# Performance work log

Hardware: AMD Instinct MI355X
Metric: run time of the kernel (lower is better)

## Reference

```python
import jax, jax.numpy as jnp
import numpy as np
from jax import lax

B, T = 512, 64
IN, H, V1, P = 256, 512, 101, 8  # input_size, rnn_size, vocab_size+1, max_param
CLS, REG = 512, 512


def setup_inputs() -> dict:
    key = jax.random.key(0)
    ks = jax.random.split(key, 20)
    u = lambda k, s: jax.random.uniform(k, s, jnp.float32, -0.1, 0.1)
    sh = 1.0 / np.sqrt(H)
    ul = lambda k, s: jax.random.uniform(k, s, jnp.float32, -sh, sh)
    return {
        "x": jax.random.normal(ks[0], (B, IN), jnp.float32),
        "y": jax.random.randint(ks[1], (B, T), 0, V1),
        "embed": u(ks[2], (V1, IN)),
        "w_ih0": ul(ks[3], (4 * H, IN)),
        "w_hh0": ul(ks[4], (4 * H, H)),
        "w_ih1": ul(ks[5], (4 * H, H)),
        "w_hh1": ul(ks[6], (4 * H, H)),
        "l1w": u(ks[7], (CLS, H)), "l1b": jnp.zeros((CLS,), jnp.float32),
        "l2w": u(ks[8], (V1, CLS)), "l2b": jnp.zeros((V1,), jnp.float32),
        "r1w": u(ks[9], (REG, H)), "r1b": jnp.zeros((REG,), jnp.float32),
        "r2w": u(ks[10], (V1 * P, V1 + REG)), "r2b": jnp.zeros((V1 * P,), jnp.float32),
    }


def _cell(xi, h, c, wih, whh):
    g = xi @ wih.T + h @ whh.T          # [B, 4H], gate order i,f,g,o (no bias)
    i, f, gg, o = jnp.split(g, 4, axis=-1)
    c = jax.nn.sigmoid(f) * c + jax.nn.sigmoid(i) * jnp.tanh(gg)
    h = jax.nn.sigmoid(o) * jnp.tanh(c)
    return h, c


def reference(x, y, embed, w_ih0, w_hh0, w_ih1, w_hh1,
              l1w, l1b, l2w, l2b, r1w, r1b, r2w, r2b):
    # teacher forcing (sample_prob=0): step-0 input is x, step-i input is embed(y[:, i-1])
    emb = embed[y[:, :-1]]                                  # [B, T-1, IN]
    xt = jnp.concatenate([x[None], jnp.transpose(emb, (1, 0, 2))], axis=0)  # [T, B, IN]

    z = jnp.zeros((x.shape[0], H), x.dtype)

    def step(carry, xi):
        h0, c0, h1, c1 = carry
        h0, c0 = _cell(xi, h0, c0, w_ih0, w_hh0)
        h1, c1 = _cell(h0, h1, c1, w_ih1, w_hh1)
        return (h0, c0, h1, c1), h1

    _, outs = lax.scan(step, (z, z, z, z), xt)              # [T, B, H]

    feat2 = jax.nn.relu(outs @ l1w.T + l1b) @ l2w.T + l2b   # [T, B, V1]
    pgm_score = jax.nn.log_softmax(feat2, axis=-1)
    trans_prob = lax.stop_gradient(jax.nn.softmax(feat2, axis=-1))
    pf1 = jax.nn.relu(outs @ r1w.T + r1b)                   # [T, B, REG]
    ps = (jnp.concatenate([trans_prob, pf1], axis=-1) @ r2w.T + r2b)
    ps = ps.reshape(T, -1, V1, P)                           # [T, B, V1, P]
    idx = y.T                                               # [T, B]
    param = ps[jnp.arange(T)[:, None], jnp.arange(x.shape[0])[None, :], idx]  # [T, B, P]
    return (jnp.transpose(pgm_score, (1, 0, 2)),            # [B, T, V1]
            jnp.transpose(param, (1, 0, 2)))                # [B, T, P]
```

## Files before the change

kernel.cpp:

```cpp
#include <hip/hip_runtime.h>
#include <stdint.h>

typedef unsigned short u16;
typedef short bf16x8 __attribute__((ext_vector_type(8)));
typedef float f32x4 __attribute__((ext_vector_type(4)));
typedef int i32x4 __attribute__((ext_vector_type(4)));

#define DEV static __device__ __forceinline__

constexpr int B_ = 512, T_ = 64, IN_ = 256, H_ = 512, V1_ = 101, P_ = 8, G4_ = 2048;
constexpr int EXR = 613;
constexpr int M_  = T_ * B_;
constexpr int NBLK = 256;

DEV float b2f(u16 u) { union { uint32_t i; float f; } v; v.i = ((uint32_t)u) << 16; return v.f; }
DEV u16 f2b(float f) {
  union { float f; uint32_t i; } v; v.f = f;
  uint32_t i = v.i;
  return (u16)((i + 0x7fffu + ((i >> 16) & 1u)) >> 16);
}
DEV float sigf(float x) { return 1.f / (1.f + __expf(-x)); }
DEV float tanh_(float x) {
  float c = fminf(fmaxf(x, -15.f), 15.f);
  float e = __expf(2.f * c);
  return (e - 1.f) / (e + 1.f);
}
DEV bf16x8 ld8(const u16* p) { return *reinterpret_cast<const bf16x8*>(p); }
DEV f32x4 mfma16(bf16x8 a, bf16x8 b, f32x4 c) {
  return __builtin_amdgcn_mfma_f32_16x16x32_bf16(a, b, c, 0, 0, 0);
}

struct CvtArgs {
  const float* src[9];
  u16* dst[9];
  int pre[10];
};

__global__ __launch_bounds__(256) void k_cvtall(CvtArgs a) {
  int gid = blockIdx.x * 256 + threadIdx.x;
  if (gid >= a.pre[9]) return;
  int s = 0;
#pragma unroll
  for (int i = 1; i < 9; ++i) s += (gid >= a.pre[i]);
  const int local = gid - a.pre[s];
  const float4 v = reinterpret_cast<const float4*>(a.src[s])[local];
  ushort4 o;
  o.x = f2b(v.x); o.y = f2b(v.y); o.z = f2b(v.z); o.w = f2b(v.w);
  reinterpret_cast<ushort4*>(a.dst[s])[local] = o;
}

__global__ __launch_bounds__(256) void k_precomp(const u16* __restrict__ ex_src,
                                                 const u16* __restrict__ wih0b,
                                                 float* __restrict__ EX0) {
  const int lane = threadIdx.x & 63;
  const int wv = threadIdx.x >> 6;
  const int m0 = blockIdx.x * 64 + wv * 16;
  const int n0 = blockIdx.y * 64;
  const int lr = lane & 15;
  const int lk = (lane >> 4) * 8;

  const int arow = m0 + lr;
  const bool valid = arow < EXR;

  f32x4 acc[4] = {};
  for (int k0 = 0; k0 < IN_; k0 += 32) {
    bf16x8 a = {};
    if (valid) a = ld8(ex_src + (size_t)arow * IN_ + k0 + lk);
#pragma unroll
    for (int c = 0; c < 4; ++c) {
      bf16x8 b = ld8(wih0b + (size_t)(n0 + c * 16 + lr) * IN_ + k0 + lk);
      acc[c] = mfma16(a, b, acc[c]);
    }
  }
  const int rb = (lane >> 4) * 4;
#pragma unroll
  for (int c = 0; c < 4; ++c)
#pragma unroll
    for (int r = 0; r < 4; ++r) {
      int row = m0 + rb + r;
      int col = n0 + c * 16 + (lane & 15);
      if (row < EXR) EX0[(size_t)row * G4_ + col] = acc[c][r];
    }
}

__global__ __launch_bounds__(512, 1) void k_scan(
    const u16* __restrict__ whh0, const u16* __restrict__ wih1, const u16* __restrict__ whh1,
    const float* __restrict__ EX0, const int* __restrict__ y,
    u16* h0buf, u16* h1buf, unsigned* flags ) {
  __shared__ u16 h0s[16 * 512];
  __shared__ u16 h1s[16 * 512];
  __shared__ u16 stage0[16][64];
  __shared__ u16 stage1[16][64];
  const size_t BH = (size_t)B_ * H_;
  const int tid = threadIdx.x;
  const int lane = tid & 63;
  const int wv = tid >> 6;
  const int q = wv & 3;
  const bool isL1 = wv >= 4;
  const int bm = blockIdx.x >> 3;
  const int bj = blockIdx.x & 7;
  const int lr = lane & 15;
  const int lk = (lane >> 4) * 8;
  const int col = bj * 64 + q * 16 + lr;
  const int rb = (lane >> 4) * 4;
  const int lcol = q * 16 + lr;

  const u16* wp[8];
#pragma unroll
  for (int g = 0; g < 4; ++g) {
    if (!isL1) {
      wp[g] = whh0 + (size_t)(g * H_ + col) * H_ + lk;
      wp[4 + g] = whh0 + (size_t)(g * H_ + col) * H_ + lk;
    } else {
      wp[g] = wih1 + (size_t)(g * H_ + col) * H_ + lk;
      wp[4 + g] = whh1 + (size_t)(g * H_ + col) * H_ + lk;
    }
  }
  f32x4 cst = {};
  unsigned* gflags = flags + bm * 16;

  for (int k = 0; k <= T_; ++k) {
    {
      const u16* h0g = h0buf + (size_t)k * BH + (size_t)(bm * 16) * H_;
#pragma unroll
      for (int rr = 0; rr < 2; ++rr) {
        const int idx = rr * 512 + tid;
        const int row = idx >> 6, cc = idx & 63;
        i32x4 d = *(const i32x4*)(h0g + (size_t)row * H_ + cc * 8);
        *(i32x4*)((char*)h0s + row * 1024 + ((cc * 16) ^ ((row & 7) << 4))) = d;
      }
      if (k >= 1) {
        const u16* h1g = h1buf + (size_t)(k - 1) * BH + (size_t)(bm * 16) * H_;
#pragma unroll
        for (int rr = 0; rr < 2; ++rr) {
          const int idx = rr * 512 + tid;
          const int row = idx >> 6, cc = idx & 63;
          i32x4 d = *(const i32x4*)(h1g + (size_t)row * H_ + cc * 8);
          *(i32x4*)((char*)h1s + row * 1024 + ((cc * 16) ^ ((row & 7) << 4))) = d;
        }
      }
    }
    __syncthreads();

    if (!isL1) {
      if (k < T_) {
        float ex[4][4];
#pragma unroll
        for (int r = 0; r < 4; ++r) {
          const int row = bm * 16 + rb + r;
          const int srow = (k == 0) ? (V1_ + row) : y[row * T_ + k - 1];
          const float* bp = EX0 + (size_t)srow * G4_ + col;
#pragma unroll
          for (int g = 0; g < 4; ++g) ex[g][r] = bp[(size_t)g * H_];
        }
        bf16x8 wf[4];
#pragma unroll
        for (int g = 0; g < 4; ++g) wf[g] = ld8(wp[g]);
        f32x4 acc[4] = {};
#pragma unroll
        for (int i = 0; i < 16; ++i) {
          bf16x8 a0 = *(const bf16x8*)((const char*)h0s + lr * 1024 + (((i * 32 + lk) * 2) ^ ((lr & 7) << 4)));
          bf16x8 nf[4];
#pragma unroll
          for (int g = 0; g < 4; ++g) nf[g] = (i < 15) ? ld8(wp[g] + (i + 1) * 32) : wf[g];
#pragma unroll
          for (int g = 0; g < 4; ++g) acc[g] = mfma16(a0, wf[g], acc[g]);
#pragma unroll
          for (int g = 0; g < 4; ++g) wf[g] = nf[g];
        }
#pragma unroll
        for (int r = 0; r < 4; ++r) {
          float iv = acc[0][r] + ex[0][r], fv = acc[1][r] + ex[1][r];
          float gv = acc[2][r] + ex[2][r], ov = acc[3][r] + ex[3][r];
          float cn = sigf(fv) * cst[r] + sigf(iv) * tanh_(gv);
          cst[r] = cn;
          stage0[rb + r][lcol] = f2b(sigf(ov) * tanh_(cn));
        }
      }
    } else {
      if (k >= 1) {
        bf16x8 wfa[4], wfb[4];
#pragma unroll
        for (int g = 0; g < 4; ++g) { wfa[g] = ld8(wp[g]); wfb[g] = ld8(wp[4 + g]); }
        f32x4 acc[4] = {};
#pragma unroll
        for (int i = 0; i < 16; ++i) {
          const int so = ((i * 32 + lk) * 2) ^ ((lr & 7) << 4);
          bf16x8 a0 = *(const bf16x8*)((const char*)h0s + lr * 1024 + so);
          bf16x8 a1 = *(const bf16x8*)((const char*)h1s + lr * 1024 + so);
          bf16x8 nfa[4], nfb[4];
#pragma unroll
          for (int g = 0; g < 4; ++g) {
            nfa[g] = (i < 15) ? ld8(wp[g] + (i + 1) * 32) : wfa[g];
            nfb[g] = (i < 15) ? ld8(wp[4 + g] + (i + 1) * 32) : wfb[g];
          }
#pragma unroll
          for (int g = 0; g < 4; ++g) {
            acc[g] = mfma16(a0, wfa[g], acc[g]);
            acc[g] = mfma16(a1, wfb[g], acc[g]);
          }
#pragma unroll
          for (int g = 0; g < 4; ++g) { wfa[g] = nfa[g]; wfb[g] = nfb[g]; }
        }
#pragma unroll
        for (int r = 0; r < 4; ++r) {
          float cn = sigf(acc[1][r]) * cst[r] + sigf(acc[0][r]) * tanh_(acc[2][r]);
          cst[r] = cn;
          stage1[rb + r][lcol] = f2b(sigf(acc[3][r]) * tanh_(cn));
        }
      }
    }
    __syncthreads();

    if (tid < 256) {
      if (tid < 128) {
        if (k < T_) {
          const int lrow = tid >> 3, c8 = (tid & 7) * 8;
          i32x4 d = *(const i32x4*)&stage0[lrow][c8];
          u16* gp = h0buf + (size_t)(k + 1) * BH + (size_t)(bm * 16 + lrow) * H_ + bj * 64 + c8;
          asm volatile("global_store_dwordx4 %0, %1, off sc0 sc1" :: "v"(gp), "v"(d) : "memory");
        }
      } else {
        if (k >= 1) {
          const int t2 = tid - 128;
          const int lrow = t2 >> 3, c8 = (t2 & 7) * 8;
          i32x4 d = *(const i32x4*)&stage1[lrow][c8];
          u16* gp = h1buf + (size_t)k * BH + (size_t)(bm * 16 + lrow) * H_ + bj * 64 + c8;
          asm volatile("global_store_dwordx4 %0, %1, off sc0 sc1" :: "v"(gp), "v"(d) : "memory");
        }
      }
    }
    asm volatile("s_waitcnt vmcnt(0)" ::: "memory");
    __syncthreads();
    if (wv == 0) {
      const unsigned tgt = (unsigned)(k + 1);
      if (lane == 0)
        __hip_atomic_store(&gflags[bj], tgt, __ATOMIC_RELAXED, __HIP_MEMORY_SCOPE_AGENT);
      for (;;) {
        unsigned v = __hip_atomic_load(&gflags[lane & 7], __ATOMIC_RELAXED, __HIP_MEMORY_SCOPE_AGENT);
        if (__all(v >= tgt)) break;
        __builtin_amdgcn_s_sleep(1);
      }
    }
    __syncthreads();
    asm volatile("" ::: "memory");
  }
}

__global__ __launch_bounds__(256) void k_fused1(const u16* __restrict__ outs,
                                                const u16* __restrict__ l1w, const float* __restrict__ l1b,
                                                const u16* __restrict__ r1w, const float* __restrict__ r1b,
                                                u16* __restrict__ feat1, u16* __restrict__ pf1) {
  const int lane = threadIdx.x & 63;
  const int wv = threadIdx.x >> 6;
  const int lr = lane & 15;
  const int lk = (lane >> 4) * 8;
  const int ar = blockIdx.x * 64 + wv * 16 + lr;
  const int rb = (lane >> 4) * 4;
  const int row0 = blockIdx.x * 64 + wv * 16 + rb;

  bf16x8 a[16];
  {
    const u16* ap = outs + (size_t)ar * H_ + lk;
#pragma unroll
    for (int i = 0; i < 16; ++i) a[i] = ld8(ap + i * 32);
  }
  for (int w = 0; w < 2; ++w) {
    const u16* W = w ? r1w : l1w;
    const float* bias = w ? r1b : l1b;
    u16* dst = w ? pf1 : feat1;
    for (int nc = 0; nc < 4; ++nc) {
      f32x4 acc[8] = {};
#pragma unroll
      for (int i = 0; i < 16; ++i)
#pragma unroll
        for (int n = 0; n < 8; ++n)
          acc[n] = mfma16(a[i], ld8(W + (size_t)(nc * 128 + n * 16 + lr) * H_ + i * 32 + lk), acc[n]);
#pragma unroll
      for (int n = 0; n < 8; ++n) {
        const int colc = nc * 128 + n * 16 + lr;
        const float bv = bias[colc];
#pragma unroll
        for (int r = 0; r < 4; ++r)
          dst[(size_t)(row0 + r) * H_ + colc] = f2b(fmaxf(acc[n][r] + bv, 0.f));
      }
    }
  }
}

__global__ __launch_bounds__(256) void k_fused2(const u16* __restrict__ feat1,
                                                const u16* __restrict__ l2w, const float* __restrict__ l2b,
                                                const u16* __restrict__ pf1,
                                                const float* __restrict__ r2w, const float* __restrict__ r2b,
                                                const int* __restrict__ y,
                                                float* __restrict__ pgm, float* __restrict__ par) {
  __shared__ float trans[64][104];
  const int lane = threadIdx.x & 63;
  const int wv = threadIdx.x >> 6;
  const int lr = lane & 15;
  const int lk = (lane >> 4) * 8;
  const int ar = blockIdx.x * 64 + wv * 16 + lr;
  const int rb = (lane >> 4) * 4;

  f32x4 acc[7] = {};
  {
    const u16* ap = feat1 + (size_t)ar * H_ + lk;
#pragma unroll
    for (int i = 0; i < 16; ++i) {
      bf16x8 av = ld8(ap + i * 32);
#pragma unroll
      for (int c = 0; c < 7; ++c) {
        const int n = c * 16 + lr;
        bf16x8 b = {};
        if (n < V1_) b = ld8(l2w + (size_t)n * H_ + i * 32 + lk);
        acc[c] = mfma16(av, b, acc[c]);
      }
    }
  }
#pragma unroll
  for (int r = 0; r < 4; ++r) {
    float v[7];
    float mx = -1e30f;
#pragma unroll
    for (int c = 0; c < 7; ++c) {
      const int colc = c * 16 + lr;
      v[c] = (colc < V1_) ? acc[c][r] + l2b[colc] : -1e30f;
      mx = fmaxf(mx, v[c]);
    }
#pragma unroll
    for (int o = 1; o < 16; o <<= 1) mx = fmaxf(mx, __shfl_xor(mx, o, 64));
    float e[7], s = 0.f;
#pragma unroll
    for (int c = 0; c < 7; ++c) { e[c] = (c * 16 + lr < V1_) ? __expf(v[c] - mx) : 0.f; s += e[c]; }
#pragma unroll
    for (int o = 1; o < 16; o <<= 1) s += __shfl_xor(s, o, 64);
    const float lz = __logf(s), inv = 1.f / s;
    const int m = blockIdx.x * 64 + wv * 16 + rb + r;
    const int t = m >> 9, bb = m & 511;
    float* po = pgm + ((size_t)bb * T_ + t) * V1_;
#pragma unroll
    for (int c = 0; c < 7; ++c) {
      const int colc = c * 16 + lr;
      if (colc < V1_) { po[colc] = v[c] - mx - lz; trans[wv * 16 + rb + r][colc] = e[c] * inv; }
    }
  }
  __syncthreads();
  for (int rr = 0; rr < 16; ++rr) {
    const int m = blockIdx.x * 64 + wv * 16 + rr;
    const int t = m >> 9, bb = m & 511;
    const int idx = y[bb * T_ + t];
    const float* wb = r2w + (size_t)idx * P_ * 613;
    float a8[P_] = {};
    for (int kk = lane; kk < 613; kk += 64) {
      float xv = (kk < V1_) ? trans[wv * 16 + rr][kk] : b2f(pf1[(size_t)m * H_ + kk - V1_]);
#pragma unroll
      for (int p = 0; p < P_; ++p) a8[p] += xv * wb[(size_t)p * 613 + kk];
    }
#pragma unroll
    for (int p = 0; p < P_; ++p)
#pragma unroll
      for (int o = 1; o < 64; o <<= 1) a8[p] += __shfl_xor(a8[p], o, 64);
    if (lane < P_) par[((size_t)bb * T_ + t) * P_ + lane] = a8[lane] + r2b[idx * P_ + lane];
  }
}

extern "C" void kernel_launch(void* const* d_in, const int* in_sizes, int n_in,
                              void* d_out, int out_size, void* d_ws, size_t ws_size,
                              hipStream_t stream) {
  (void)in_sizes; (void)n_in; (void)out_size; (void)ws_size;
  const float* x     = (const float*)d_in[0];
  const int*   y     = (const int*)d_in[1];
  const float* embed = (const float*)d_in[2];
  const float* wih0  = (const float*)d_in[3];
  const float* whh0  = (const float*)d_in[4];
  const float* wih1  = (const float*)d_in[5];
  const float* whh1  = (const float*)d_in[6];
  const float* l1w   = (const float*)d_in[7];
  const float* l1b   = (const float*)d_in[8];
  const float* l2w   = (const float*)d_in[9];
  const float* l2b   = (const float*)d_in[10];
  const float* r1w   = (const float*)d_in[11];
  const float* r1b   = (const float*)d_in[12];
  const float* r2w   = (const float*)d_in[13];
  const float* r2b   = (const float*)d_in[14];

  float* out_pgm = (float*)d_out;
  float* out_par = out_pgm + (size_t)B_ * T_ * V1_;

  char* ws = (char*)d_ws;
  size_t off = 0;
  auto alloc = [&](size_t bytes) { void* p = ws + off; off += (bytes + 255) & ~(size_t)255; return p; };

  const size_t BH2 = (size_t)B_ * H_ * 2;

  unsigned* flags = (unsigned*)alloc(32 * 16 * 4);
  u16* h0buf  = (u16*)alloc((size_t)(T_ + 1) * BH2);
  u16* h1buf  = (u16*)alloc((size_t)(T_ + 1) * BH2);

  float* EX0   = (float*)alloc((size_t)EXR * G4_ * 4);
  u16* ex_src  = (u16*)alloc((size_t)EXR * IN_ * 2);
  u16* wih0b   = (u16*)alloc((size_t)4 * H_ * IN_ * 2);
  u16* whh0b   = (u16*)alloc((size_t)4 * H_ * H_ * 2);
  u16* wih1b   = (u16*)alloc((size_t)4 * H_ * H_ * 2);
  u16* whh1b   = (u16*)alloc((size_t)4 * H_ * H_ * 2);
  u16* l1wb    = (u16*)alloc((size_t)H_ * H_ * 2);
  u16* r1wb    = (u16*)alloc((size_t)H_ * H_ * 2);
  u16* l2wb    = (u16*)alloc((size_t)V1_ * H_ * 2);
  u16* feat1   = (u16*)alloc((size_t)M_ * H_ * 2);
  u16* pf1     = (u16*)alloc((size_t)M_ * H_ * 2);

  (void)hipMemsetAsync(flags, 0, 32 * 16 * 4 + BH2, stream);
  (void)hipMemsetAsync(h1buf, 0, BH2, stream);

  CvtArgs ca;
  const float* srcs[9] = {embed, x, wih0, whh0, wih1, whh1, l1w, r1w, l2w};
  u16* dsts[9] = {ex_src, ex_src + (size_t)V1_ * IN_, wih0b, whh0b, wih1b, whh1b, l1wb, r1wb, l2wb};
  int ns[9] = {V1_ * IN_, B_ * IN_, 4 * H_ * IN_, 4 * H_ * H_, 4 * H_ * H_, 4 * H_ * H_,
               H_ * H_, H_ * H_, V1_ * H_};
  int acc4 = 0;
  for (int i = 0; i < 9; ++i) {
    ca.src[i] = srcs[i]; ca.dst[i] = dsts[i]; ca.pre[i] = acc4; acc4 += ns[i] / 4;
  }
  ca.pre[9] = acc4;
  k_cvtall<<<(acc4 + 255) / 256, 256, 0, stream>>>(ca);

  k_precomp<<<dim3(10, 32), 256, 0, stream>>>(ex_src, wih0b, EX0);

  k_scan<<<NBLK, 512, 0, stream>>>(whh0b, wih1b, whh1b, EX0, y, h0buf, h1buf, flags);

  u16* outs = h1buf + (size_t)B_ * H_;
  k_fused1<<<512, 256, 0, stream>>>(outs, l1wb, l1b, r1wb, r1b, feat1, pf1);
  k_fused2<<<512, 256, 0, stream>>>(feat1, l2wb, l2b, pf1, r2w, r2b, y, out_pgm, out_par);
}
```

Before: 1.934 ms.

## Split scan blocks by LSTM layer and pipeline layers with per-layer flags

```diff
diff --git a/kernel.cpp b/kernel.cpp
--- a/kernel.cpp
+++ b/kernel.cpp
@@ -11,7 +11,6 @@
 constexpr int B_ = 512, T_ = 64, IN_ = 256, H_ = 512, V1_ = 101, P_ = 8, G4_ = 2048;
 constexpr int EXR = 613;
 constexpr int M_  = T_ * B_;
-constexpr int NBLK = 256;
 
 DEV float b2f(u16 u) { union { uint32_t i; float f; } v; v.i = ((uint32_t)u) << 16; return v.f; }
 DEV u16 f2b(float f) {
@@ -26,6 +25,9 @@
   return (e - 1.f) / (e + 1.f);
 }
 DEV bf16x8 ld8(const u16* p) { return *reinterpret_cast<const bf16x8*>(p); }
+DEV i32x4 ld16nt(const void* p) {
+  return __builtin_nontemporal_load(reinterpret_cast<const i32x4*>(p));
+}
 DEV f32x4 mfma16(bf16x8 a, bf16x8 b, f32x4 c) {
   return __builtin_amdgcn_mfma_f32_16x16x32_bf16(a, b, c, 0, 0, 0);
 }
@@ -86,164 +88,170 @@
 __global__ __launch_bounds__(512, 1) void k_scan(
     const u16* __restrict__ whh0, const u16* __restrict__ wih1, const u16* __restrict__ whh1,
     const float* __restrict__ EX0, const int* __restrict__ y,
-    u16* h0buf, u16* h1buf, unsigned* flags ) {
+    u16* h0loc, u16* h0pub, u16* h1buf,
+    unsigned* flags ) {
   __shared__ u16 h0s[16 * 512];
   __shared__ u16 h1s[16 * 512];
-  __shared__ u16 stage0[16][64];
-  __shared__ u16 stage1[16][64];
+  __shared__ u16 stg[16 * 128];
   const size_t BH = (size_t)B_ * H_;
   const int tid = threadIdx.x;
   const int lane = tid & 63;
   const int wv = tid >> 6;
-  const int q = wv & 3;
-  const bool isL1 = wv >= 4;
-  const int bm = blockIdx.x >> 3;
-  const int bj = blockIdx.x & 7;
+  const int x_ = blockIdx.x & 7;
+  const int j  = blockIdx.x >> 3;
+  const bool isL1 = x_ >= 4;
+  const int rg = (x_ & 3) * 8 + (j & 7);
+  const int cs = j >> 3;
+  const int row0 = rg * 16;
   const int lr = lane & 15;
   const int lk = (lane >> 4) * 8;
-  const int col = bj * 64 + q * 16 + lr;
   const int rb = (lane >> 4) * 4;
-  const int lcol = q * 16 + lr;
-
-  const u16* wp[8];
+  const int col = cs * 128 + wv * 16 + lr;
+  const int lcol = wv * 16 + lr;
+
+  const u16* wpa[4]; const u16* wpb[4];
 #pragma unroll
   for (int g = 0; g < 4; ++g) {
+    wpa[g] = (isL1 ? wih1 : whh0) + (size_t)(g * H_ + col) * H_ + lk;
+    wpb[g] = whh1 + (size_t)(g * H_ + col) * H_ + lk;
+  }
+  f32x4 cst = {};
+  unsigned* f0 = flags + rg * 32;
+  unsigned* f1 = flags + 1024 + rg * 32;
+
+  for (int k = 0; k < T_; ++k) {
+    if (wv == 0 && (k > 0 || isL1)) {
+      const unsigned* ap = nullptr; unsigned thr = 0;
+      if (!isL1) {
+        if (lane < 4) { ap = f0 + lane; thr = (unsigned)k; }
+      } else {
+        if (lane < 4)      { ap = f0 + lane;     thr = (unsigned)(k + 1); }
+        else if (lane < 8) { ap = f1 + lane - 4; thr = (unsigned)k; }
+      }
+      for (;;) {
+        unsigned v = 0xffffffffu;
+        if (ap) v = __hip_atomic_load(ap, __ATOMIC_RELAXED, __HIP_MEMORY_SCOPE_AGENT);
+        if (__all(v >= thr)) break;
+        __builtin_amdgcn_s_sleep(1);
+      }
+    }
+    __syncthreads();
+
     if (!isL1) {
-      wp[g] = whh0 + (size_t)(g * H_ + col) * H_ + lk;
-      wp[4 + g] = whh0 + (size_t)(g * H_ + col) * H_ + lk;
-    } else {
-      wp[g] = wih1 + (size_t)(g * H_ + col) * H_ + lk;
-      wp[4 + g] = whh1 + (size_t)(g * H_ + col) * H_ + lk;
-    }
-  }
-  f32x4 cst = {};
-  unsigned* gflags = flags + bm * 16;
-
-  for (int k = 0; k <= T_; ++k) {
-    {
-      const u16* h0g = h0buf + (size_t)k * BH + (size_t)(bm * 16) * H_;
+      const u16* src = h0loc + (size_t)k * BH + (size_t)row0 * H_;
 #pragma unroll
       for (int rr = 0; rr < 2; ++rr) {
         const int idx = rr * 512 + tid;
         const int row = idx >> 6, cc = idx & 63;
-        i32x4 d = *(const i32x4*)(h0g + (size_t)row * H_ + cc * 8);
+        i32x4 d = *(const i32x4*)(src + (size_t)row * H_ + cc * 8);
         *(i32x4*)((char*)h0s + row * 1024 + ((cc * 16) ^ ((row & 7) << 4))) = d;
       }
-      if (k >= 1) {
-        const u16* h1g = h1buf + (size_t)(k - 1) * BH + (size_t)(bm * 16) * H_;
-#pragma unroll
-        for (int rr = 0; rr < 2; ++rr) {
-          const int idx = rr * 512 + tid;
-          const int row = idx >> 6, cc = idx & 63;
-          i32x4 d = *(const i32x4*)(h1g + (size_t)row * H_ + cc * 8);
-          *(i32x4*)((char*)h1s + row * 1024 + ((cc * 16) ^ ((row & 7) << 4))) = d;
+    } else {
+      const u16* s0 = h0pub + (size_t)(k + 1) * BH + (size_t)row0 * H_;
+      const u16* s1 = h1buf + (size_t)k * BH + (size_t)row0 * H_;
+#pragma unroll
+      for (int rr = 0; rr < 2; ++rr) {
+        const int idx = rr * 512 + tid;
+        const int row = idx >> 6, cc = idx & 63;
+        i32x4 d0 = ld16nt(s0 + (size_t)row * H_ + cc * 8);
+        *(i32x4*)((char*)h0s + row * 1024 + ((cc * 16) ^ ((row & 7) << 4))) = d0;
+        i32x4 d1 = *(const i32x4*)(s1 + (size_t)row * H_ + cc * 8);
+        *(i32x4*)((char*)h1s + row * 1024 + ((cc * 16) ^ ((row & 7) << 4))) = d1;
+      }
+    }
+    __syncthreads();
+
+    if (!isL1) {
+      float ex[4][4];
+#pragma unroll
+      for (int r = 0; r < 4; ++r) {
+        const int row = row0 + rb + r;
+        const int srow = (k == 0) ? (V1_ + row) : y[row * T_ + k - 1];
+        const float* bp = EX0 + (size_t)srow * G4_ + col;
+#pragma unroll
+        for (int g = 0; g < 4; ++g) ex[g][r] = bp[(size_t)g * H_];
+      }
+      bf16x8 wf[4];
+#pragma unroll
+      for (int g = 0; g < 4; ++g) wf[g] = ld8(wpa[g]);
+      f32x4 acc[4] = {};
+#pragma unroll
+      for (int i = 0; i < 16; ++i) {
+        bf16x8 a0 = *(const bf16x8*)((const char*)h0s + lr * 1024 + (((i * 32 + lk) * 2) ^ ((lr & 7) << 4)));
+        bf16x8 nf[4];
+#pragma unroll
+        for (int g = 0; g < 4; ++g) nf[g] = (i < 15) ? ld8(wpa[g] + (i + 1) * 32) : wf[g];
+#pragma unroll
+        for (int g = 0; g < 4; ++g) acc[g] = mfma16(a0, wf[g], acc[g]);
+#pragma unroll
+        for (int g = 0; g < 4; ++g) wf[g] = nf[g];
+      }
+#pragma unroll
+      for (int r = 0; r < 4; ++r) {
+        float iv = acc[0][r] + ex[0][r], fv = acc[1][r] + ex[1][r];
+        float gv = acc[2][r] + ex[2][r], ov = acc[3][r] + ex[3][r];
+        float cn = sigf(fv) * cst[r] + sigf(iv) * tanh_(gv);
+        cst[r] = cn;
+        stg[(rb + r) * 128 + lcol] = f2b(sigf(ov) * tanh_(cn));
+      }
+    } else {
+      bf16x8 wfa[4], wfb[4];
+#pragma unroll
+      for (int g = 0; g < 4; ++g) { wfa[g] = ld8(wpa[g]); wfb[g] = ld8(wpb[g]); }
+      f32x4 acc[4] = {};
+#pragma unroll
+      for (int i = 0; i < 16; ++i) {
+        const int so = ((i * 32 + lk) * 2) ^ ((lr & 7) << 4);
+        bf16x8 a0 = *(const bf16x8*)((const char*)h0s + lr * 1024 + so);
+        bf16x8 a1 = *(const bf16x8*)((const char*)h1s + lr * 1024 + so);
+        bf16x8 nfa[4], nfb[4];
+#pragma unroll
+        for (int g = 0; g < 4; ++g) {
+          nfa[g] = (i < 15) ? ld8(wpa[g] + (i + 1) * 32) : wfa[g];
+          nfb[g] = (i < 15) ? ld8(wpb[g] + (i + 1) * 32) : wfb[g];
         }
+#pragma unroll
+        for (int g = 0; g < 4; ++g) {
+          acc[g] = mfma16(a0, wfa[g], acc[g]);
+          acc[g] = mfma16(a1, wfb[g], acc[g]);
+        }
+#pragma unroll
+        for (int g = 0; g < 4; ++g) { wfa[g] = nfa[g]; wfb[g] = nfb[g]; }
+      }
+#pragma unroll
+      for (int r = 0; r < 4; ++r) {
+        float cn = sigf(acc[1][r]) * cst[r] + sigf(acc[0][r]) * tanh_(acc[2][r]);
+        cst[r] = cn;
+        stg[(rb + r) * 128 + lcol] = f2b(sigf(acc[3][r]) * tanh_(cn));
       }
     }
     __syncthreads();
 
     if (!isL1) {
-      if (k < T_) {
-        float ex[4][4];
-#pragma unroll
-        for (int r = 0; r < 4; ++r) {
-          const int row = bm * 16 + rb + r;
-          const int srow = (k == 0) ? (V1_ + row) : y[row * T_ + k - 1];
-          const float* bp = EX0 + (size_t)srow * G4_ + col;
-#pragma unroll
-          for (int g = 0; g < 4; ++g) ex[g][r] = bp[(size_t)g * H_];
-        }
-        bf16x8 wf[4];
-#pragma unroll
-        for (int g = 0; g < 4; ++g) wf[g] = ld8(wp[g]);
-        f32x4 acc[4] = {};
-#pragma unroll
-        for (int i = 0; i < 16; ++i) {
-          bf16x8 a0 = *(const bf16x8*)((const char*)h0s + lr * 1024 + (((i * 32 + lk) * 2) ^ ((lr & 7) << 4)));
-          bf16x8 nf[4];
-#pragma unroll
-          for (int g = 0; g < 4; ++g) nf[g] = (i < 15) ? ld8(wp[g] + (i + 1) * 32) : wf[g];
-#pragma unroll
-          for (int g = 0; g < 4; ++g) acc[g] = mfma16(a0, wf[g], acc[g]);
-#pragma unroll
-          for (int g = 0; g < 4; ++g) wf[g] = nf[g];
-        }
-#pragma unroll
-        for (int r = 0; r < 4; ++r) {
-          float iv = acc[0][r] + ex[0][r], fv = acc[1][r] + ex[1][r];
-          float gv = acc[2][r] + ex[2][r], ov = acc[3][r] + ex[3][r];
-          float cn = sigf(fv) * cst[r] + sigf(iv) * tanh_(gv);
-          cst[r] = cn;
-          stage0[rb + r][lcol] = f2b(sigf(ov) * tanh_(cn));
-        }
+      if (tid < 256) {
+        const int r = tid >> 4, c8 = (tid & 15) * 8;
+        i32x4 d = *(const i32x4*)&stg[r * 128 + c8];
+        *(i32x4*)(h0loc + (size_t)(k + 1) * BH + (size_t)(row0 + r) * H_ + cs * 128 + c8) = d;
+      } else {
+        const int t2 = tid - 256;
+        const int r = t2 >> 4, c8 = (t2 & 15) * 8;
+        i32x4 d = *(const i32x4*)&stg[r * 128 + c8];
+        u16* gp = h0pub + (size_t)(k + 1) * BH + (size_t)(row0 + r) * H_ + cs * 128 + c8;
+        asm volatile("global_store_dwordx4 %0, %1, off sc0 sc1" :: "v"(gp), "v"(d) : "memory");
       }
     } else {
-      if (k >= 1) {
-        bf16x8 wfa[4], wfb[4];
-#pragma unroll
-        for (int g = 0; g < 4; ++g) { wfa[g] = ld8(wp[g]); wfb[g] = ld8(wp[4 + g]); }
-        f32x4 acc[4] = {};
-#pragma unroll
-        for (int i = 0; i < 16; ++i) {
-          const int so = ((i * 32 + lk) * 2) ^ ((lr & 7) << 4);
-          bf16x8 a0 = *(const bf16x8*)((const char*)h0s + lr * 1024 + so);
-          bf16x8 a1 = *(const bf16x8*)((const char*)h1s + lr * 1024 + so);
-          bf16x8 nfa[4], nfb[4];
-#pragma unroll
-          for (int g = 0; g < 4; ++g) {
-            nfa[g] = (i < 15) ? ld8(wp[g] + (i + 1) * 32) : wfa[g];
-            nfb[g] = (i < 15) ? ld8(wp[4 + g] + (i + 1) * 32) : wfb[g];
-          }
-#pragma unroll
-          for (int g = 0; g < 4; ++g) {
-            acc[g] = mfma16(a0, wfa[g], acc[g]);
-            acc[g] = mfma16(a1, wfb[g], acc[g]);
-          }
-#pragma unroll
-          for (int g = 0; g < 4; ++g) { wfa[g] = nfa[g]; wfb[g] = nfb[g]; }
-        }
-#pragma unroll
-        for (int r = 0; r < 4; ++r) {
-          float cn = sigf(acc[1][r]) * cst[r] + sigf(acc[0][r]) * tanh_(acc[2][r]);
-          cst[r] = cn;
-          stage1[rb + r][lcol] = f2b(sigf(acc[3][r]) * tanh_(cn));
-        }
-      }
-    }
-    __syncthreads();
-
-    if (tid < 256) {
-      if (tid < 128) {
-        if (k < T_) {
-          const int lrow = tid >> 3, c8 = (tid & 7) * 8;
-          i32x4 d = *(const i32x4*)&stage0[lrow][c8];
-          u16* gp = h0buf + (size_t)(k + 1) * BH + (size_t)(bm * 16 + lrow) * H_ + bj * 64 + c8;
-          asm volatile("global_store_dwordx4 %0, %1, off sc0 sc1" :: "v"(gp), "v"(d) : "memory");
-        }
-      } else {
-        if (k >= 1) {
-          const int t2 = tid - 128;
-          const int lrow = t2 >> 3, c8 = (t2 & 7) * 8;
-          i32x4 d = *(const i32x4*)&stage1[lrow][c8];
-          u16* gp = h1buf + (size_t)k * BH + (size_t)(bm * 16 + lrow) * H_ + bj * 64 + c8;
-          asm volatile("global_store_dwordx4 %0, %1, off sc0 sc1" :: "v"(gp), "v"(d) : "memory");
-        }
+      if (tid < 256) {
+        const int r = tid >> 4, c8 = (tid & 15) * 8;
+        i32x4 d = *(const i32x4*)&stg[r * 128 + c8];
+        *(i32x4*)(h1buf + (size_t)(k + 1) * BH + (size_t)(row0 + r) * H_ + cs * 128 + c8) = d;
       }
     }
     asm volatile("s_waitcnt vmcnt(0)" ::: "memory");
     __syncthreads();
-    if (wv == 0) {
-      const unsigned tgt = (unsigned)(k + 1);
-      if (lane == 0)
-        __hip_atomic_store(&gflags[bj], tgt, __ATOMIC_RELAXED, __HIP_MEMORY_SCOPE_AGENT);
-      for (;;) {
-        unsigned v = __hip_atomic_load(&gflags[lane & 7], __ATOMIC_RELAXED, __HIP_MEMORY_SCOPE_AGENT);
-        if (__all(v >= tgt)) break;
-        __builtin_amdgcn_s_sleep(1);
-      }
-    }
-    __syncthreads();
-    asm volatile("" ::: "memory");
+    if (tid == 0) {
+      unsigned* fa = isL1 ? (f1 + cs) : (f0 + cs);
+      __hip_atomic_store(fa, (unsigned)(k + 1), __ATOMIC_RELAXED, __HIP_MEMORY_SCOPE_AGENT);
+    }
   }
 }
 
@@ -393,8 +401,9 @@
 
   const size_t BH2 = (size_t)B_ * H_ * 2;
 
-  unsigned* flags = (unsigned*)alloc(32 * 16 * 4);
-  u16* h0buf  = (u16*)alloc((size_t)(T_ + 1) * BH2);
+  unsigned* flags = (unsigned*)alloc(8192);
+  u16* h0loc  = (u16*)alloc((size_t)(T_ + 1) * BH2);
+  u16* h0pub  = (u16*)alloc((size_t)(T_ + 1) * BH2);
   u16* h1buf  = (u16*)alloc((size_t)(T_ + 1) * BH2);
 
   float* EX0   = (float*)alloc((size_t)EXR * G4_ * 4);
@@ -409,7 +418,7 @@
   u16* feat1   = (u16*)alloc((size_t)M_ * H_ * 2);
   u16* pf1     = (u16*)alloc((size_t)M_ * H_ * 2);
 
-  (void)hipMemsetAsync(flags, 0, 32 * 16 * 4 + BH2, stream);
+  (void)hipMemsetAsync(flags, 0, 8192 + BH2, stream);
   (void)hipMemsetAsync(h1buf, 0, BH2, stream);
 
   CvtArgs ca;
@@ -426,7 +435,7 @@
 
   k_precomp<<<dim3(10, 32), 256, 0, stream>>>(ex_src, wih0b, EX0);
 
-  k_scan<<<NBLK, 512, 0, stream>>>(whh0b, wih1b, whh1b, EX0, y, h0buf, h1buf, flags);
+  k_scan<<<256, 512, 0, stream>>>(whh0b, wih1b, whh1b, EX0, y, h0loc, h0pub, h1buf, flags);
 
   u16* outs = h1buf + (size_t)B_ * H_;
   k_fused1<<<512, 256, 0, stream>>>(outs, l1wb, l1b, r1wb, r1b, feat1, pf1);
```

Measured after the change: 2.329 ms. 1.2x slower.
